# Performance work log

Measured on AMD Instinct MI355X. Metric: run time of the kernel, lower is better.

Reference implementation:

```python
import jax, jax.numpy as jnp
import numpy as np

B, L, H, NH, DH = 2, 4096, 768, 12, 64
W_ = 128          # one-sided sliding window
NL = 2            # encoder layers
VOCAB, OUT, FF = 50265, 384, 3072
EPS = 1e-5


def _ln(x, s, b):
    m = jnp.mean(x, axis=-1, keepdims=True)
    v = jnp.mean((x - m) ** 2, axis=-1, keepdims=True)
    return (x - m) / jnp.sqrt(v + EPS) * s + b


def _attn(x, amask, Wq, bq, Wk, bk, Wv, bv, Wo, bo):
    # x: [B,L,H]; sliding-window attention (one-sided W_) + global token 0
    def heads(Wt, bt):
        return (x @ Wt + bt).reshape(B, L, NH, DH).transpose(0, 2, 1, 3)  # [B,NH,L,DH]
    q, k, v = heads(Wq, bq), heads(Wk, bk), heads(Wv, bv)
    scale = 1.0 / np.sqrt(DH).astype(np.float32)
    C = W_
    nC = L // C
    qc = q.reshape(B, NH, nC, C, DH)

    def blocks(t):  # gather [prev, self, next] key chunks -> [B,NH,nC,3C,DH]
        tc = t.reshape(B, NH, nC, C, DH)
        tp = jnp.pad(tc, ((0, 0), (0, 0), (1, 1), (0, 0), (0, 0)))
        return jnp.concatenate([tp[:, :, :-2], tp[:, :, 1:-1], tp[:, :, 2:]], axis=3)

    k3, v3 = blocks(k), blocks(v)
    s_loc = jnp.einsum('bhncd,bhnkd->bhnck', qc, k3) * scale  # [B,NH,nC,C,3C]

    pos_k = (jnp.arange(nC)[:, None] - 1) * C + jnp.arange(3 * C)[None, :]  # [nC,3C]
    pos_q = jnp.arange(nC)[:, None] * C + jnp.arange(C)[None, :]            # [nC,C]
    within = jnp.abs(pos_q[:, :, None] - pos_k[:, None, :]) <= W_           # [nC,C,3C]
    valid = (pos_k >= 0) & (pos_k < L) & (pos_k != 0)  # key 0 handled as global column
    mk = amask[:, jnp.clip(pos_k, 0, L - 1)] > 0        # [B,nC,3C]
    m = within[None, None] & valid[None, None, :, None, :] & mk[:, None, :, None, :]
    s_loc = jnp.where(m, s_loc, -1e9)

    # every token also attends to the global token 0
    s_g = jnp.einsum('bhld,bhd->bhl', q, k[:, :, 0]) * scale  # [B,NH,L]
    s = jnp.concatenate([s_loc.reshape(B, NH, L, 3 * C), s_g[..., None]], axis=-1)
    p = jax.nn.softmax(s, axis=-1)
    p_loc = p[..., :3 * C].reshape(B, NH, nC, C, 3 * C)
    out = jnp.einsum('bhnck,bhnkd->bhncd', p_loc, v3).reshape(B, NH, L, DH)
    out = out + p[..., -1:] * v[:, :, 0][:, :, None, :]

    # global token 0 attends to everything
    s0 = jnp.einsum('bhd,bhld->bhl', q[:, :, 0], k) * scale
    s0 = jnp.where(amask[:, None, :] > 0, s0, -1e9)
    o0 = jnp.einsum('bhl,bhld->bhd', jax.nn.softmax(s0, axis=-1), v)
    out = out.at[:, :, 0, :].set(o0)

    out = out.transpose(0, 2, 1, 3).reshape(B, L, H)
    return out @ Wo + bo


def setup_inputs() -> dict:
    key = jax.random.key(0)
    ks = jax.random.split(key, 16)
    p = lambda k_, sh: 0.02 * jax.random.normal(k_, sh, jnp.float32)
    return {
        'input_ids': jax.random.randint(ks[0], (B, L), 0, VOCAB, dtype=jnp.int32),
        'attention_mask': jnp.ones((B, L), jnp.int32),
        'word_emb': p(ks[1], (VOCAB, H)),
        'pos_emb': p(ks[2], (L, H)),
        'emb_ln_s': jnp.ones((H,), jnp.float32), 'emb_ln_b': jnp.zeros((H,), jnp.float32),
        'Wq': p(ks[3], (NL, H, H)), 'bq': jnp.zeros((NL, H), jnp.float32),
        'Wk': p(ks[4], (NL, H, H)), 'bk': jnp.zeros((NL, H), jnp.float32),
        'Wv': p(ks[5], (NL, H, H)), 'bv': jnp.zeros((NL, H), jnp.float32),
        'Wo': p(ks[6], (NL, H, H)), 'bo': jnp.zeros((NL, H), jnp.float32),
        'ln1_s': jnp.ones((NL, H), jnp.float32), 'ln1_b': jnp.zeros((NL, H), jnp.float32),
        'W1': p(ks[7], (NL, H, FF)), 'b1': jnp.zeros((NL, FF), jnp.float32),
        'W2': p(ks[8], (NL, FF, H)), 'b2': jnp.zeros((NL, H), jnp.float32),
        'ln2_s': jnp.ones((NL, H), jnp.float32), 'ln2_b': jnp.zeros((NL, H), jnp.float32),
        'Wfc': p(ks[9], (H, OUT)), 'bfc': jnp.zeros((OUT,), jnp.float32),
    }


def reference(input_ids, attention_mask, word_emb, pos_emb, emb_ln_s, emb_ln_b,
              Wq, bq, Wk, bk, Wv, bv, Wo, bo, ln1_s, ln1_b,
              W1, b1, W2, b2, ln2_s, ln2_b, Wfc, bfc):
    x = word_emb[input_ids] + pos_emb[None]
    x = _ln(x, emb_ln_s, emb_ln_b)
    for l in range(NL):
        a = _attn(x, attention_mask, Wq[l], bq[l], Wk[l], bk[l], Wv[l], bv[l], Wo[l], bo[l])
        x = _ln(x + a, ln1_s[l], ln1_b[l])
        h = jax.nn.gelu(x @ W1[l] + b1[l])
        x = _ln(x + h @ W2[l] + b2[l], ln2_s[l], ln2_b[l])
    v_dn = x @ Wfc + bfc           # [B,L,OUT]
    cls = v_dn[:, 0]               # fc(last_hidden[:,0]) == v_dn[:,0]
    return v_dn, cls
```

## Files before the change

### kernel.cpp

```cpp
#include <hip/hip_runtime.h>
#include <hip/hip_bf16.h>
#include <stdint.h>

#define L_SEQ 4096
#define H_DIM 768
#define N_HEADS 12
#define D_HEAD 64
#define N_CHUNK 32
#define CHUNK 128
#define FF_DIM 3072
#define OUT_DIM 384
#define BATCH 2
#define EPS_LN 1e-5f
#define M_ROWS (BATCH * L_SEQ)
#define QKV_LD (3 * H_DIM)
#define NLOC (BATCH * N_HEADS * N_CHUNK)
#define NGSEG 8

typedef unsigned short u16;
typedef __bf16 bx8 __attribute__((ext_vector_type(8)));
typedef float fx4 __attribute__((ext_vector_type(4)));
typedef u16 ux8 __attribute__((ext_vector_type(8)));

__device__ __forceinline__ u16 f2bf(float f) {
  union { float f; unsigned u; } x; x.f = f;
  unsigned r = x.u + 0x7fffu + ((x.u >> 16) & 1u);
  return (u16)(r >> 16);
}
__device__ __forceinline__ float bf2f(u16 v) {
  union { unsigned u; float f; } x; x.u = ((unsigned)v) << 16;
  return x.f;
}

__device__ __forceinline__ void gload16(const void* g, void* l) {
  __builtin_amdgcn_global_load_lds((const __attribute__((address_space(1))) void*)g,
                                   (__attribute__((address_space(3))) void*)l, 16, 0, 0);
}

template<int OUT_BF16, int DO_GELU, int DO_CLS>
__global__ __launch_bounds__(256, 3)
void gemm_s(const u16* __restrict__ A, const u16* __restrict__ Bt,
            const float* __restrict__ bias,
            float* __restrict__ Cf, u16* __restrict__ Cb,
            float* __restrict__ cls,
            int N, int K)
{
  __shared__ __align__(16) u16 As[128 * 64];
  __shared__ __align__(16) u16 Bs[128 * 64];
  const int tid = threadIdx.x;
  const int lane = tid & 63, w = tid >> 6;
  const int c16 = lane & 15, g = lane >> 4;
  const int wr = w >> 1, wc = w & 1;

  const int nbn = N >> 7;
  int id = blockIdx.x;
  id = (id & 7) * (gridDim.x >> 3) + (id >> 3);
  const int bm = id / nbn, bn = id % nbn;

  const int srow = w * 8 + (lane >> 3);
  const int schunk = (lane & 7) ^ (lane >> 3);
  const u16* sA = A + (size_t)(bm * 128 + srow) * K + schunk * 8;
  const u16* sB = Bt + (size_t)(bn * 128 + srow) * K + schunk * 8;
  const int wdst = w * 512;

  fx4 acc[4][4] = {};

  for (int k0 = 0; k0 < K; k0 += 64) {
    #pragma unroll
    for (int i = 0; i < 4; i++) {
      gload16(sA + (size_t)(i * 32) * K + k0, &As[i * 2048 + wdst]);
      gload16(sB + (size_t)(i * 32) * K + k0, &Bs[i * 2048 + wdst]);
    }
    __syncthreads();
    #pragma unroll
    for (int h = 0; h < 2; h++) {
      bx8 af[4], bf[4];
      #pragma unroll
      for (int m = 0; m < 4; m++) {
        const int row = wr * 64 + m * 16 + c16;
        af[m] = *(const bx8*)&As[row * 64 + (((h << 2) + g) ^ (c16 & 7)) * 8];
      }
      #pragma unroll
      for (int n = 0; n < 4; n++) {
        const int row = wc * 64 + n * 16 + c16;
        bf[n] = *(const bx8*)&Bs[row * 64 + (((h << 2) + g) ^ (c16 & 7)) * 8];
      }
      #pragma unroll
      for (int m = 0; m < 4; m++)
        #pragma unroll
        for (int n = 0; n < 4; n++)
          acc[m][n] = __builtin_amdgcn_mfma_f32_16x16x32_bf16(af[m], bf[n], acc[m][n], 0, 0, 0);
    }
    __syncthreads();
  }

  const int row0 = bm * 128 + wr * 64 + g * 4;
  const int col0 = bn * 128 + wc * 64 + c16;
  #pragma unroll
  for (int n = 0; n < 4; n++) {
    const int col = col0 + n * 16;
    const float bb = bias[col];
    #pragma unroll
    for (int m = 0; m < 4; m++) {
      #pragma unroll
      for (int r = 0; r < 4; r++) {
        float y = acc[m][n][r] + bb;
        if (DO_GELU) {
          const float tt = y;
          y = 0.5f * tt * (1.0f + tanhf(0.7978845608f * (tt + 0.044715f * tt * tt * tt)));
        }
        const int row = row0 + m * 16 + r;
        const size_t idx = (size_t)row * N + col;
        if (OUT_BF16) Cb[idx] = f2bf(y);
        else Cf[idx] = y;
        if (DO_CLS) {
          if ((row & (L_SEQ - 1)) == 0)
            cls[(row >> 12) * OUT_DIM + col] = y;
        }
      }
    }
  }
}

#define P2_STR 64

__global__ __launch_bounds__(512, 2)
void attn_fused_kernel(const u16* __restrict__ qkv, const int* __restrict__ amask,
                       u16* __restrict__ attnout,
                       float* __restrict__ gpm, float* __restrict__ gps,
                       float* __restrict__ gpo)
{
  __shared__ __align__(16) u16 Klds[2][64 * 64];
  __shared__ __align__(16) u16 Vlds[2][64 * 64];
  __shared__ __align__(16) u16 Plds[8 * 16 * P2_STR];

  const int tid = threadIdx.x;
  const int lane = tid & 63, w = tid >> 6;

  if (blockIdx.x >= NLOC) {
    float* fsc = (float*)&Klds[0][0];
    float* qs  = fsc;
    float* es  = fsc + 64;
    float* red = fsc + 576;
    const int idx = blockIdx.x - NLOC;
    const int bh = idx >> 3, seg = idx & 7;
    const int b = bh / N_HEADS, h = bh % N_HEADS;
    const u16* base = qkv + (size_t)b * L_SEQ * QKV_LD + h * D_HEAD;

    if (tid < D_HEAD) qs[tid] = bf2f(base[tid]);
    __syncthreads();

    const int key = seg * 512 + tid;
    const ux8* kp = (const ux8*)(base + (size_t)key * QKV_LD + H_DIM);
    float dot = 0.f;
    #pragma unroll
    for (int i = 0; i < 8; i++) {
      const ux8 kv = kp[i];
      #pragma unroll
      for (int j = 0; j < 8; j++) dot += qs[i * 8 + j] * bf2f(kv[j]);
    }
    float sv = dot * 0.125f;
    if (amask[b * L_SEQ + key] == 0) sv = -1.0e9f;

    float mv = sv;
    #pragma unroll
    for (int off = 32; off > 0; off >>= 1) mv = fmaxf(mv, __shfl_xor(mv, off));
    if (lane == 0) red[w] = mv;
    __syncthreads();
    float M = -3.0e38f;
    #pragma unroll
    for (int i = 0; i < 8; i++) M = fmaxf(M, red[i]);

    const float e = __expf(sv - M);
    es[tid] = e;
    float s = e;
    #pragma unroll
    for (int off = 32; off > 0; off >>= 1) s += __shfl_xor(s, off);
    __syncthreads();
    if (lane == 0) red[w] = s;
    __syncthreads();
    float Sl = 0.f;
    #pragma unroll
    for (int i = 0; i < 8; i++) Sl += red[i];

    const int gi = tid >> 6, d = lane;
    const u16* vb = base + 2 * H_DIM + d;
    float acc = 0.f;
    #pragma unroll 4
    for (int i = 0; i < 64; i++) {
      const int kk = seg * 512 + gi * 64 + i;
      acc += es[gi * 64 + i] * bf2f(vb[(size_t)kk * QKV_LD]);
    }
    gpo[(((size_t)bh * NGSEG + seg) * 8 + gi) * D_HEAD + d] = acc;
    if (tid == 0) { gpm[bh * NGSEG + seg] = M; gps[bh * NGSEG + seg] = Sl; }
    return;
  }

  const int c16 = lane & 15, g = lane >> 4;
  const int bh = blockIdx.x >> 5;
  const int n = blockIdx.x & 31;
  const int b = bh / N_HEADS, h = bh % N_HEADS;

  const u16* qkvb = qkv + (size_t)b * L_SEQ * QKV_LD + h * D_HEAD;
  const int chunk_lo = n * CHUNK - CHUNK;

  const int qrow = n * CHUNK + w * 16 + c16;
  const u16* qp = qkvb + (size_t)qrow * QKV_LD + g * 8;
  const bx8 aq0 = *(const bx8*)qp;
  const bx8 aq1 = *(const bx8*)(qp + 32);

  unsigned kvm = 0;
  #pragma unroll
  for (int kf = 0; kf < 24; kf++) {
    const int pos = chunk_lo + kf * 16 + c16;
    bool ok = (pos >= 1) && (pos < L_SEQ);
    if (ok) ok = (amask[b * L_SEQ + pos] > 0);
    kvm |= ((unsigned)ok) << kf;
  }

  const int cq = w * 16 + g * 4;

  float m[4], l[4], pgv[4];
  {
    const u16* kp = qkvb + H_DIM + g * 8;
    const bx8 b0 = *(const bx8*)kp;
    const bx8 b1 = *(const bx8*)(kp + 32);
    fx4 sg = {};
    sg = __builtin_amdgcn_mfma_f32_16x16x32_bf16(aq0, b0, sg, 0, 0, 0);
    sg = __builtin_amdgcn_mfma_f32_16x16x32_bf16(aq1, b1, sg, 0, 0, 0);
    #pragma unroll
    for (int r = 0; r < 4; r++) {
      const float val = (c16 == 0) ? sg[r] * 0.125f : -1.0e9f;
      float mm = val;
      mm = fmaxf(mm, __shfl_xor(mm, 1));
      mm = fmaxf(mm, __shfl_xor(mm, 2));
      mm = fmaxf(mm, __shfl_xor(mm, 4));
      mm = fmaxf(mm, __shfl_xor(mm, 8));
      m[r] = mm;
      pgv[r] = __expf(val - mm);
      float t = pgv[r];
      t += __shfl_xor(t, 1);
      t += __shfl_xor(t, 2);
      t += __shfl_xor(t, 4);
      t += __shfl_xor(t, 8);
      l[r] = t;
    }
  }

  const int krow_s = w * 8 + (lane >> 3);
  const int ksc = (lane & 7) ^ (krow_s & 7);
  const int d = lane;
  const int vdst = d * 64 + ((w ^ (d & 7)) << 3);

  {
    int pos = chunk_lo + krow_s;
    if (pos < 0) pos = 0;
    if (pos >= L_SEQ) pos = L_SEQ - 1;
    gload16(qkvb + (size_t)pos * QKV_LD + H_DIM + ksc * 8, &Klds[0][w * 512]);
  }
  ux8 vreg;
  #pragma unroll
  for (int j = 0; j < 8; j++) {
    int pos = chunk_lo + w * 8 + j;
    if (pos < 0) pos = 0;
    if (pos >= L_SEQ) pos = L_SEQ - 1;
    vreg[j] = qkvb[(size_t)pos * QKV_LD + 2 * H_DIM + d];
  }
  *(ux8*)&Vlds[0][vdst] = vreg;
  __syncthreads();

  fx4 o[4] = {};
  u16* pb = Plds + w * 16 * P2_STR;
  const int prow = (w * 16 + c16) * P2_STR;

  for (int t = 0; t < 6; t++) {
    const int cur = t & 1, nxt = cur ^ 1;

    if (t < 5) {
      int pos = chunk_lo + (t + 1) * 64 + krow_s;
      if (pos < 0) pos = 0;
      if (pos >= L_SEQ) pos = L_SEQ - 1;
      gload16(qkvb + (size_t)pos * QKV_LD + H_DIM + ksc * 8, &Klds[nxt][w * 512]);
      #pragma unroll
      for (int j = 0; j < 8; j++) {
        int vp = chunk_lo + (t + 1) * 64 + w * 8 + j;
        if (vp < 0) vp = 0;
        if (vp >= L_SEQ) vp = L_SEQ - 1;
        vreg[j] = qkvb[(size_t)vp * QKV_LD + 2 * H_DIM + d];
      }
    }

    fx4 s[4];
    __builtin_amdgcn_s_setprio(1);
    #pragma unroll
    for (int kf = 0; kf < 4; kf++) {
      const int krow = kf * 16 + c16;
      const bx8 b0 = *(const bx8*)&Klds[cur][krow * 64 + ((g ^ (c16 & 7)) << 3)];
      const bx8 b1 = *(const bx8*)&Klds[cur][krow * 64 + (((4 + g) ^ (c16 & 7)) << 3)];
      fx4 a = {};
      a = __builtin_amdgcn_mfma_f32_16x16x32_bf16(aq0, b0, a, 0, 0, 0);
      a = __builtin_amdgcn_mfma_f32_16x16x32_bf16(aq1, b1, a, 0, 0, 0);
      s[kf] = a;
    }
    __builtin_amdgcn_s_setprio(0);
    float pmax[4];
    #pragma unroll
    for (int r = 0; r < 4; r++) pmax[r] = -3.0e38f;
    #pragma unroll
    for (int kf = 0; kf < 4; kf++) {
      const int KF = t * 4 + kf;
      const int j = KF * 16 + c16;
      const bool kv = ((kvm >> KF) & 1u) != 0;
      #pragma unroll
      for (int r = 0; r < 4; r++) {
        const int c = cq + r;
        const bool keep = kv && (j >= c && j <= c + 256);
        const float val = keep ? s[kf][r] * 0.125f : -1.0e9f;
        s[kf][r] = val;
        pmax[r] = fmaxf(pmax[r], val);
      }
    }
    #pragma unroll
    for (int r = 0; r < 4; r++) {
      float mm = pmax[r];
      mm = fmaxf(mm, __shfl_xor(mm, 1));
      mm = fmaxf(mm, __shfl_xor(mm, 2));
      mm = fmaxf(mm, __shfl_xor(mm, 4));
      mm = fmaxf(mm, __shfl_xor(mm, 8));
      const float newm = fmaxf(m[r], mm);
      const float scale = __expf(m[r] - newm);
      m[r] = newm;
      l[r] *= scale;
      pgv[r] *= scale;
      #pragma unroll
      for (int df = 0; df < 4; df++) o[df][r] *= scale;
    }
    float lsum[4] = {0.f, 0.f, 0.f, 0.f};
    #pragma unroll
    for (int kf = 0; kf < 4; kf++)
      #pragma unroll
      for (int r = 0; r < 4; r++) {
        const float p = __expf(s[kf][r] - m[r]);
        s[kf][r] = p;
        lsum[r] += p;
      }
    #pragma unroll
    for (int r = 0; r < 4; r++) {
      float tt = lsum[r];
      tt += __shfl_xor(tt, 1);
      tt += __shfl_xor(tt, 2);
      tt += __shfl_xor(tt, 4);
      tt += __shfl_xor(tt, 8);
      l[r] += tt;
    }
    #pragma unroll
    for (int kf = 0; kf < 4; kf++) {
      #pragma unroll
      for (int r = 0; r < 4; r++) {
        const int rr = g * 4 + r;
        const int jj = kf * 16 + c16;
        pb[rr * P2_STR + (((jj >> 3) ^ (rr & 7)) << 3) + (jj & 7)] = f2bf(s[kf][r]);
      }
    }
    __builtin_amdgcn_s_setprio(1);
    #pragma unroll
    for (int kt = 0; kt < 2; kt++) {
      const int ckp = kt * 4 + g;
      const bx8 pa = *(const bx8*)&Plds[prow + ((ckp ^ (c16 & 7)) << 3)];
      #pragma unroll
      for (int df = 0; df < 4; df++) {
        const int vrow = df * 16 + c16;
        const bx8 vvf = *(const bx8*)&Vlds[cur][vrow * 64 + ((ckp ^ (c16 & 7)) << 3)];
        o[df] = __builtin_amdgcn_mfma_f32_16x16x32_bf16(pa, vvf, o[df], 0, 0, 0);
      }
    }
    __builtin_amdgcn_s_setprio(0);
    if (t < 5) *(ux8*)&Vlds[nxt][vdst] = vreg;
    __syncthreads();
  }

  float rinv[4], pg[4];
  #pragma unroll
  for (int r = 0; r < 4; r++) {
    rinv[r] = 1.0f / l[r];
    pg[r] = __shfl(pgv[r], g * 16);
  }
  u16* ob = attnout + (size_t)b * L_SEQ * H_DIM + h * D_HEAD;
  const int posq = n * CHUNK + w * 16 + g * 4;
  #pragma unroll
  for (int df = 0; df < 4; df++) {
    const float v0f = bf2f(qkvb[2 * H_DIM + df * 16 + c16]);
    #pragma unroll
    for (int r = 0; r < 4; r++)
      ob[(size_t)(posq + r) * H_DIM + df * 16 + c16] =
          f2bf((o[df][r] + pg[r] * v0f) * rinv[r]);
  }
}

__global__ __launch_bounds__(64)
void attn_g_combine(const float* __restrict__ gpm, const float* __restrict__ gps,
                    const float* __restrict__ gpo, u16* __restrict__ attnout)
{
  const int bh = blockIdx.x;
  const int b = bh / N_HEADS, h = bh % N_HEADS;
  const int d = threadIdx.x;
  float M = -3.0e38f;
  #pragma unroll
  for (int s = 0; s < NGSEG; s++) M = fmaxf(M, gpm[bh * NGSEG + s]);
  float S = 0.f, acc = 0.f;
  #pragma unroll
  for (int s = 0; s < NGSEG; s++) {
    const float sc = __expf(gpm[bh * NGSEG + s] - M);
    S += gps[bh * NGSEG + s] * sc;
    #pragma unroll
    for (int gi = 0; gi < 8; gi++)
      acc += gpo[(((size_t)bh * NGSEG + s) * 8 + gi) * D_HEAD + d] * sc;
  }
  attnout[(size_t)b * L_SEQ * H_DIM + h * D_HEAD + d] = f2bf(acc / S);
}

__device__ __forceinline__ void block_stats(float sum, float sq, float* red,
                                            float& mean, float& rstd)
{
  const int lane = threadIdx.x & 63, wv = threadIdx.x >> 6;
  #pragma unroll
  for (int off = 32; off > 0; off >>= 1) {
    sum += __shfl_xor(sum, off);
    sq  += __shfl_xor(sq, off);
  }
  if (lane == 0) { red[wv] = sum; red[4 + wv] = sq; }
  __syncthreads();
  sum = red[0] + red[1] + red[2] + red[3];
  sq  = red[4] + red[5] + red[6] + red[7];
  mean = sum * (1.0f / H_DIM);
  const float var = sq * (1.0f / H_DIM) - mean * mean;
  rstd = rsqrtf(var + EPS_LN);
}

__global__ __launch_bounds__(256)
void add_ln_kernel(u16* xio, const u16* __restrict__ yin,
                   const float* __restrict__ gam, const float* __restrict__ bet)
{
  __shared__ float red[8];
  const int row = blockIdx.x, tid = threadIdx.x;
  float v[3]; float sum = 0.f, sq = 0.f;
  #pragma unroll
  for (int i = 0; i < 3; i++) {
    const int c = tid + i * 256;
    const float t = bf2f(xio[(size_t)row * H_DIM + c]) + bf2f(yin[(size_t)row * H_DIM + c]);
    v[i] = t; sum += t; sq += t * t;
  }
  float mean, rstd;
  block_stats(sum, sq, red, mean, rstd);
  #pragma unroll
  for (int i = 0; i < 3; i++) {
    const int c = tid + i * 256;
    const float y = (v[i] - mean) * rstd * gam[c] + bet[c];
    xio[(size_t)row * H_DIM + c] = f2bf(y);
  }
}

__global__ __launch_bounds__(256)
void prep_embed(const float* __restrict__ Wq, const float* __restrict__ Wk,
                const float* __restrict__ Wv, const float* __restrict__ Wo,
                const float* __restrict__ W1, const float* __restrict__ W2,
                const float* __restrict__ Wfc,
                const float* __restrict__ bq, const float* __restrict__ bk,
                const float* __restrict__ bv,
                u16* __restrict__ wqkvT, u16* __restrict__ woT,
                u16* __restrict__ w1T, u16* __restrict__ w2T,
                u16* __restrict__ wfcT, float* __restrict__ bqkv,
                const int* __restrict__ ids, const float* __restrict__ wemb,
                const float* __restrict__ pemb, const float* __restrict__ gam,
                const float* __restrict__ bet, u16* __restrict__ xb)
{
  const int t = blockIdx.x;
  const int tid = threadIdx.x;
  __shared__ float tile[32][33];

  if (t >= 14130) {
    const int row = t - 14130;
    const int l = row & (L_SEQ - 1);
    const int id = ids[row];
    float v[3]; float sum = 0.f, sq = 0.f;
    #pragma unroll
    for (int i = 0; i < 3; i++) {
      const int c = tid + i * 256;
      const float x = wemb[(size_t)id * H_DIM + c] + pemb[(size_t)l * H_DIM + c];
      v[i] = x; sum += x; sq += x * x;
    }
    float mean, rstd;
    block_stats(sum, sq, &tile[0][0], mean, rstd);
    #pragma unroll
    for (int i = 0; i < 3; i++) {
      const int c = tid + i * 256;
      const float y = (v[i] - mean) * rstd * gam[c] + bet[c];
      xb[(size_t)row * H_DIM + c] = f2bf(y);
    }
    return;
  }
  if (t >= 14112) {
    const int idx = t - 14112;
    const int l = idx / 9, j = idx % 9;
    const int i = j * 256 + tid;
    if (i < H_DIM)          bqkv[l * QKV_LD + i] = bq[l * H_DIM + i];
    else if (i < 2 * H_DIM) bqkv[l * QKV_LD + i] = bk[l * H_DIM + i - H_DIM];
    else if (i < 3 * H_DIM) bqkv[l * QKV_LD + i] = bv[l * H_DIM + i - 2 * H_DIM];
    return;
  }
  const float* src; u16* dst; int K, N, r;
  if (t < 13824) {
    const int l = t / 6912; r = t % 6912;
    if (r < 2304) {
      const int mq = r / 576; r = r % 576; K = H_DIM; N = H_DIM;
      if (mq == 0)      src = Wq + (size_t)l * H_DIM * H_DIM;
      else if (mq == 1) src = Wk + (size_t)l * H_DIM * H_DIM;
      else if (mq == 2) src = Wv + (size_t)l * H_DIM * H_DIM;
      else              src = Wo + (size_t)l * H_DIM * H_DIM;
      dst = (mq < 3) ? wqkvT + (size_t)l * QKV_LD * H_DIM + (size_t)mq * H_DIM * H_DIM
                     : woT + (size_t)l * H_DIM * H_DIM;
    } else if (r < 4608) {
      r -= 2304; K = H_DIM; N = FF_DIM;
      src = W1 + (size_t)l * H_DIM * FF_DIM;
      dst = w1T + (size_t)l * FF_DIM * H_DIM;
    } else {
      r -= 4608; K = FF_DIM; N = H_DIM;
      src = W2 + (size_t)l * FF_DIM * H_DIM;
      dst = w2T + (size_t)l * H_DIM * FF_DIM;
    }
  } else {
    r = t - 13824; K = H_DIM; N = OUT_DIM; src = Wfc; dst = wfcT;
  }
  const int ntn = N >> 5;
  const int k0 = (r / ntn) * 32, n0 = (r % ntn) * 32;
  const int tx = tid & 31, ty = tid >> 5;
  #pragma unroll
  for (int i = 0; i < 32; i += 8)
    tile[ty + i][tx] = src[(size_t)(k0 + ty + i) * N + n0 + tx];
  __syncthreads();
  #pragma unroll
  for (int i = 0; i < 32; i += 8)
    dst[(size_t)(n0 + ty + i) * K + k0 + tx] = f2bf(tile[tx][ty + i]);
}

extern "C" void kernel_launch(void* const* d_in, const int* in_sizes, int n_in,
                              void* d_out, int out_size, void* d_ws, size_t ws_size,
                              hipStream_t stream)
{
  (void)in_sizes; (void)n_in; (void)out_size; (void)ws_size;
  const int*   ids   = (const int*)d_in[0];
  const int*   amask = (const int*)d_in[1];
  const float* wemb  = (const float*)d_in[2];
  const float* pemb  = (const float*)d_in[3];
  const float* elns  = (const float*)d_in[4];
  const float* elnb  = (const float*)d_in[5];
  const float* Wq    = (const float*)d_in[6];
  const float* bq    = (const float*)d_in[7];
  const float* Wk    = (const float*)d_in[8];
  const float* bk    = (const float*)d_in[9];
  const float* Wv    = (const float*)d_in[10];
  const float* bv    = (const float*)d_in[11];
  const float* Wo    = (const float*)d_in[12];
  const float* bo    = (const float*)d_in[13];
  const float* ln1s  = (const float*)d_in[14];
  const float* ln1b  = (const float*)d_in[15];
  const float* W1    = (const float*)d_in[16];
  const float* b1    = (const float*)d_in[17];
  const float* W2    = (const float*)d_in[18];
  const float* b2    = (const float*)d_in[19];
  const float* ln2s  = (const float*)d_in[20];
  const float* ln2b  = (const float*)d_in[21];
  const float* Wfc   = (const float*)d_in[22];
  const float* bfc   = (const float*)d_in[23];

  char* ws = (char*)d_ws;
  size_t off = 0;
  auto alloc = [&](size_t bytes) -> void* {
    void* p = ws + off;
    off += (bytes + 255) & ~(size_t)255;
    return p;
  };
  u16* xb     = (u16*)alloc((size_t)M_ROWS * H_DIM * 2);
  u16* projb  = (u16*)alloc((size_t)M_ROWS * H_DIM * 2);
  u16* big    = (u16*)alloc((size_t)M_ROWS * FF_DIM * 2);
  u16* attno  = (u16*)alloc((size_t)M_ROWS * H_DIM * 2);
  u16* wqkvT  = (u16*)alloc((size_t)2 * QKV_LD * H_DIM * 2);
  u16* woT    = (u16*)alloc((size_t)2 * H_DIM * H_DIM * 2);
  u16* w1T    = (u16*)alloc((size_t)2 * FF_DIM * H_DIM * 2);
  u16* w2T    = (u16*)alloc((size_t)2 * H_DIM * FF_DIM * 2);
  u16* wfcT   = (u16*)alloc((size_t)OUT_DIM * H_DIM * 2);
  float* bqkv = (float*)alloc(2 * QKV_LD * 4);
  float* gpm  = (float*)alloc((size_t)BATCH * N_HEADS * NGSEG * 4);
  float* gps  = (float*)alloc((size_t)BATCH * N_HEADS * NGSEG * 4);
  float* gpo  = (float*)alloc((size_t)BATCH * N_HEADS * NGSEG * 8 * D_HEAD * 4);

  u16* qkvb = big;
  u16* ff1  = big;

  prep_embed<<<14130 + M_ROWS, 256, 0, stream>>>(
      Wq, Wk, Wv, Wo, W1, W2, Wfc, bq, bk, bv,
      wqkvT, woT, w1T, w2T, wfcT, bqkv,
      ids, wemb, pemb, elns, elnb, xb);

  for (int l = 0; l < 2; l++) {
    gemm_s<1, 0, 0><<<(M_ROWS / 128) * (QKV_LD / 128), 256, 0, stream>>>(
        xb, wqkvT + (size_t)l * QKV_LD * H_DIM, bqkv + l * QKV_LD,
        nullptr, qkvb, nullptr, QKV_LD, H_DIM);
    attn_fused_kernel<<<NLOC + BATCH * N_HEADS * NGSEG, 512, 0, stream>>>(
        qkvb, amask, attno, gpm, gps, gpo);
    attn_g_combine<<<BATCH * N_HEADS, 64, 0, stream>>>(gpm, gps, gpo, attno);
    gemm_s<1, 0, 0><<<(M_ROWS / 128) * (H_DIM / 128), 256, 0, stream>>>(
        attno, woT + (size_t)l * H_DIM * H_DIM, bo + l * H_DIM,
        nullptr, projb, nullptr, H_DIM, H_DIM);
    add_ln_kernel<<<M_ROWS, 256, 0, stream>>>(xb, projb, ln1s + l * H_DIM, ln1b + l * H_DIM);
    gemm_s<1, 1, 0><<<(M_ROWS / 128) * (FF_DIM / 128), 256, 0, stream>>>(
        xb, w1T + (size_t)l * FF_DIM * H_DIM, b1 + l * FF_DIM,
        nullptr, ff1, nullptr, FF_DIM, H_DIM);
    gemm_s<1, 0, 0><<<(M_ROWS / 128) * (H_DIM / 128), 256, 0, stream>>>(
        ff1, w2T + (size_t)l * H_DIM * FF_DIM, b2 + l * H_DIM,
        nullptr, projb, nullptr, H_DIM, FF_DIM);
    add_ln_kernel<<<M_ROWS, 256, 0, stream>>>(xb, projb, ln2s + l * H_DIM, ln2b + l * H_DIM);
  }

  float* vdn = (float*)d_out;
  float* cls = vdn + (size_t)BATCH * L_SEQ * OUT_DIM;
  gemm_s<0, 0, 1><<<(M_ROWS / 128) * (OUT_DIM / 128), 256, 0, stream>>>(
      xb, wfcT, bfc, vdn, nullptr, cls, OUT_DIM, H_DIM);
}
```

Measured before the change: 591.8 us.

## Split fused attention and prep kernels, raise GEMM occupancy hint

```diff
diff --git a/kernel.cpp b/kernel.cpp
--- a/kernel.cpp
+++ b/kernel.cpp
@@ -14,7 +14,6 @@
 #define EPS_LN 1e-5f
 #define M_ROWS (BATCH * L_SEQ)
 #define QKV_LD (3 * H_DIM)
-#define NLOC (BATCH * N_HEADS * N_CHUNK)
 #define NGSEG 8
 
 typedef unsigned short u16;
@@ -38,7 +37,7 @@
 }
 
 template<int OUT_BF16, int DO_GELU, int DO_CLS>
-__global__ __launch_bounds__(256, 3)
+__global__ __launch_bounds__(256, 4)
 void gemm_s(const u16* __restrict__ A, const u16* __restrict__ Bt,
             const float* __restrict__ bias,
             float* __restrict__ Cf, u16* __restrict__ Cb,
@@ -125,10 +124,8 @@
 #define P2_STR 64
 
 __global__ __launch_bounds__(512, 2)
-void attn_fused_kernel(const u16* __restrict__ qkv, const int* __restrict__ amask,
-                       u16* __restrict__ attnout,
-                       float* __restrict__ gpm, float* __restrict__ gps,
-                       float* __restrict__ gpo)
+void attn_local_kernel(const u16* __restrict__ qkv, const int* __restrict__ amask,
+                       u16* __restrict__ attnout)
 {
   __shared__ __align__(16) u16 Klds[2][64 * 64];
   __shared__ __align__(16) u16 Vlds[2][64 * 64];
@@ -136,67 +133,8 @@
 
   const int tid = threadIdx.x;
   const int lane = tid & 63, w = tid >> 6;
-
-  if (blockIdx.x >= NLOC) {
-    float* fsc = (float*)&Klds[0][0];
-    float* qs  = fsc;
-    float* es  = fsc + 64;
-    float* red = fsc + 576;
-    const int idx = blockIdx.x - NLOC;
-    const int bh = idx >> 3, seg = idx & 7;
-    const int b = bh / N_HEADS, h = bh % N_HEADS;
-    const u16* base = qkv + (size_t)b * L_SEQ * QKV_LD + h * D_HEAD;
-
-    if (tid < D_HEAD) qs[tid] = bf2f(base[tid]);
-    __syncthreads();
-
-    const int key = seg * 512 + tid;
-    const ux8* kp = (const ux8*)(base + (size_t)key * QKV_LD + H_DIM);
-    float dot = 0.f;
-    #pragma unroll
-    for (int i = 0; i < 8; i++) {
-      const ux8 kv = kp[i];
-      #pragma unroll
-      for (int j = 0; j < 8; j++) dot += qs[i * 8 + j] * bf2f(kv[j]);
-    }
-    float sv = dot * 0.125f;
-    if (amask[b * L_SEQ + key] == 0) sv = -1.0e9f;
-
-    float mv = sv;
-    #pragma unroll
-    for (int off = 32; off > 0; off >>= 1) mv = fmaxf(mv, __shfl_xor(mv, off));
-    if (lane == 0) red[w] = mv;
-    __syncthreads();
-    float M = -3.0e38f;
-    #pragma unroll
-    for (int i = 0; i < 8; i++) M = fmaxf(M, red[i]);
-
-    const float e = __expf(sv - M);
-    es[tid] = e;
-    float s = e;
-    #pragma unroll
-    for (int off = 32; off > 0; off >>= 1) s += __shfl_xor(s, off);
-    __syncthreads();
-    if (lane == 0) red[w] = s;
-    __syncthreads();
-    float Sl = 0.f;
-    #pragma unroll
-    for (int i = 0; i < 8; i++) Sl += red[i];
-
-    const int gi = tid >> 6, d = lane;
-    const u16* vb = base + 2 * H_DIM + d;
-    float acc = 0.f;
-    #pragma unroll 4
-    for (int i = 0; i < 64; i++) {
-      const int kk = seg * 512 + gi * 64 + i;
-      acc += es[gi * 64 + i] * bf2f(vb[(size_t)kk * QKV_LD]);
-    }
-    gpo[(((size_t)bh * NGSEG + seg) * 8 + gi) * D_HEAD + d] = acc;
-    if (tid == 0) { gpm[bh * NGSEG + seg] = M; gps[bh * NGSEG + seg] = Sl; }
-    return;
-  }
-
   const int c16 = lane & 15, g = lane >> 4;
+
   const int bh = blockIdx.x >> 5;
   const int n = blockIdx.x & 31;
   const int b = bh / N_HEADS, h = bh % N_HEADS;
@@ -397,6 +335,69 @@
   }
 }
 
+__global__ __launch_bounds__(512)
+void attn_g_split(const u16* __restrict__ qkv, const int* __restrict__ amask,
+                  float* __restrict__ gpm, float* __restrict__ gps,
+                  float* __restrict__ gpo)
+{
+  __shared__ float qs[D_HEAD];
+  __shared__ float es[512];
+  __shared__ float red[8];
+  const int tid = threadIdx.x;
+  const int lane = tid & 63, w = tid >> 6;
+  const int idx = blockIdx.x;
+  const int bh = idx >> 3, seg = idx & 7;
+  const int b = bh / N_HEADS, h = bh % N_HEADS;
+  const u16* base = qkv + (size_t)b * L_SEQ * QKV_LD + h * D_HEAD;
+
+  if (tid < D_HEAD) qs[tid] = bf2f(base[tid]);
+  __syncthreads();
+
+  const int key = seg * 512 + tid;
+  const ux8* kp = (const ux8*)(base + (size_t)key * QKV_LD + H_DIM);
+  float dot = 0.f;
+  #pragma unroll
+  for (int i = 0; i < 8; i++) {
+    const ux8 kv = kp[i];
+    #pragma unroll
+    for (int j = 0; j < 8; j++) dot += qs[i * 8 + j] * bf2f(kv[j]);
+  }
+  float sv = dot * 0.125f;
+  if (amask[b * L_SEQ + key] == 0) sv = -1.0e9f;
+
+  float mv = sv;
+  #pragma unroll
+  for (int off = 32; off > 0; off >>= 1) mv = fmaxf(mv, __shfl_xor(mv, off));
+  if (lane == 0) red[w] = mv;
+  __syncthreads();
+  float M = -3.0e38f;
+  #pragma unroll
+  for (int i = 0; i < 8; i++) M = fmaxf(M, red[i]);
+
+  const float e = __expf(sv - M);
+  es[tid] = e;
+  float s = e;
+  #pragma unroll
+  for (int off = 32; off > 0; off >>= 1) s += __shfl_xor(s, off);
+  __syncthreads();
+  if (lane == 0) red[w] = s;
+  __syncthreads();
+  float Sl = 0.f;
+  #pragma unroll
+  for (int i = 0; i < 8; i++) Sl += red[i];
+
+  const int gi = tid >> 6, d = lane;
+  const u16* vb = base + 2 * H_DIM + d;
+  float acc = 0.f;
+  #pragma unroll 4
+  for (int i = 0; i < 64; i++) {
+    const int kk = seg * 512 + gi * 64 + i;
+    acc += es[gi * 64 + i] * bf2f(vb[(size_t)kk * QKV_LD]);
+  }
+  gpo[(((size_t)bh * NGSEG + seg) * 8 + gi) * D_HEAD + d] = acc;
+  if (tid == 0) { gpm[bh * NGSEG + seg] = M; gps[bh * NGSEG + seg] = Sl; }
+}
+
 __global__ __launch_bounds__(64)
 void attn_g_combine(const float* __restrict__ gpm, const float* __restrict__ gps,
                     const float* __restrict__ gpo, u16* __restrict__ attnout)
@@ -438,6 +439,32 @@
 }
 
 __global__ __launch_bounds__(256)
+void embed_ln_kernel(const int* __restrict__ ids, const float* __restrict__ wemb,
+                     const float* __restrict__ pemb, const float* __restrict__ gam,
+                     const float* __restrict__ bet, u16* __restrict__ xb)
+{
+  __shared__ float red[8];
+  const int row = blockIdx.x, tid = threadIdx.x;
+  const int l = row & (L_SEQ - 1);
+  const int id = ids[row];
+  float v[3]; float sum = 0.f, sq = 0.f;
+  #pragma unroll
+  for (int i = 0; i < 3; i++) {
+    const int c = tid + i * 256;
+    const float t = wemb[(size_t)id * H_DIM + c] + pemb[(size_t)l * H_DIM + c];
+    v[i] = t; sum += t; sq += t * t;
+  }
+  float mean, rstd;
+  block_stats(sum, sq, red, mean, rstd);
+  #pragma unroll
+  for (int i = 0; i < 3; i++) {
+    const int c = tid + i * 256;
+    const float y = (v[i] - mean) * rstd * gam[c] + bet[c];
+    xb[(size_t)row * H_DIM + c] = f2bf(y);
+  }
+}
+
+__global__ __launch_bounds__(256)
 void add_ln_kernel(u16* xio, const u16* __restrict__ yin,
                    const float* __restrict__ gam, const float* __restrict__ bet)
 {
@@ -461,44 +488,18 @@
 }
 
 __global__ __launch_bounds__(256)
-void prep_embed(const float* __restrict__ Wq, const float* __restrict__ Wk,
-                const float* __restrict__ Wv, const float* __restrict__ Wo,
-                const float* __restrict__ W1, const float* __restrict__ W2,
-                const float* __restrict__ Wfc,
-                const float* __restrict__ bq, const float* __restrict__ bk,
-                const float* __restrict__ bv,
-                u16* __restrict__ wqkvT, u16* __restrict__ woT,
-                u16* __restrict__ w1T, u16* __restrict__ w2T,
-                u16* __restrict__ wfcT, float* __restrict__ bqkv,
-                const int* __restrict__ ids, const float* __restrict__ wemb,
-                const float* __restrict__ pemb, const float* __restrict__ gam,
-                const float* __restrict__ bet, u16* __restrict__ xb)
+void prep_weights(const float* __restrict__ Wq, const float* __restrict__ Wk,
+                  const float* __restrict__ Wv, const float* __restrict__ Wo,
+                  const float* __restrict__ W1, const float* __restrict__ W2,
+                  const float* __restrict__ Wfc,
+                  const float* __restrict__ bq, const float* __restrict__ bk,
+                  const float* __restrict__ bv,
+                  u16* __restrict__ wqkvT, u16* __restrict__ woT,
+                  u16* __restrict__ w1T, u16* __restrict__ w2T,
+                  u16* __restrict__ wfcT, float* __restrict__ bqkv)
 {
   const int t = blockIdx.x;
   const int tid = threadIdx.x;
-  __shared__ float tile[32][33];
-
-  if (t >= 14130) {
-    const int row = t - 14130;
-    const int l = row & (L_SEQ - 1);
-    const int id = ids[row];
-    float v[3]; float sum = 0.f, sq = 0.f;
-    #pragma unroll
-    for (int i = 0; i < 3; i++) {
-      const int c = tid + i * 256;
-      const float x = wemb[(size_t)id * H_DIM + c] + pemb[(size_t)l * H_DIM + c];
-      v[i] = x; sum += x; sq += x * x;
-    }
-    float mean, rstd;
-    block_stats(sum, sq, &tile[0][0], mean, rstd);
-    #pragma unroll
-    for (int i = 0; i < 3; i++) {
-      const int c = tid + i * 256;
-      const float y = (v[i] - mean) * rstd * gam[c] + bet[c];
-      xb[(size_t)row * H_DIM + c] = f2bf(y);
-    }
-    return;
-  }
   if (t >= 14112) {
     const int idx = t - 14112;
     const int l = idx / 9, j = idx % 9;
@@ -512,13 +513,13 @@
   if (t < 13824) {
     const int l = t / 6912; r = t % 6912;
     if (r < 2304) {
-      const int mq = r / 576; r = r % 576; K = H_DIM; N = H_DIM;
-      if (mq == 0)      src = Wq + (size_t)l * H_DIM * H_DIM;
-      else if (mq == 1) src = Wk + (size_t)l * H_DIM * H_DIM;
-      else if (mq == 2) src = Wv + (size_t)l * H_DIM * H_DIM;
-      else              src = Wo + (size_t)l * H_DIM * H_DIM;
-      dst = (mq < 3) ? wqkvT + (size_t)l * QKV_LD * H_DIM + (size_t)mq * H_DIM * H_DIM
-                     : woT + (size_t)l * H_DIM * H_DIM;
+      const int m = r / 576; r = r % 576; K = H_DIM; N = H_DIM;
+      if (m == 0)      src = Wq + (size_t)l * H_DIM * H_DIM;
+      else if (m == 1) src = Wk + (size_t)l * H_DIM * H_DIM;
+      else if (m == 2) src = Wv + (size_t)l * H_DIM * H_DIM;
+      else             src = Wo + (size_t)l * H_DIM * H_DIM;
+      dst = (m < 3) ? wqkvT + (size_t)l * QKV_LD * H_DIM + (size_t)m * H_DIM * H_DIM
+                    : woT + (size_t)l * H_DIM * H_DIM;
     } else if (r < 4608) {
       r -= 2304; K = H_DIM; N = FF_DIM;
       src = W1 + (size_t)l * H_DIM * FF_DIM;
@@ -533,6 +534,7 @@
   }
   const int ntn = N >> 5;
   const int k0 = (r / ntn) * 32, n0 = (r % ntn) * 32;
+  __shared__ float tile[32][33];
   const int tx = tid & 31, ty = tid >> 5;
   #pragma unroll
   for (int i = 0; i < 32; i += 8)
@@ -597,17 +599,17 @@
   u16* qkvb = big;
   u16* ff1  = big;
 
-  prep_embed<<<14130 + M_ROWS, 256, 0, stream>>>(
-      Wq, Wk, Wv, Wo, W1, W2, Wfc, bq, bk, bv,
-      wqkvT, woT, w1T, w2T, wfcT, bqkv,
-      ids, wemb, pemb, elns, elnb, xb);
+  prep_weights<<<14130, 256, 0, stream>>>(Wq, Wk, Wv, Wo, W1, W2, Wfc,
+                                          bq, bk, bv,
+                                          wqkvT, woT, w1T, w2T, wfcT, bqkv);
+  embed_ln_kernel<<<M_ROWS, 256, 0, stream>>>(ids, wemb, pemb, elns, elnb, xb);
 
   for (int l = 0; l < 2; l++) {
     gemm_s<1, 0, 0><<<(M_ROWS / 128) * (QKV_LD / 128), 256, 0, stream>>>(
         xb, wqkvT + (size_t)l * QKV_LD * H_DIM, bqkv + l * QKV_LD,
         nullptr, qkvb, nullptr, QKV_LD, H_DIM);
-    attn_fused_kernel<<<NLOC + BATCH * N_HEADS * NGSEG, 512, 0, stream>>>(
-        qkvb, amask, attno, gpm, gps, gpo);
+    attn_local_kernel<<<BATCH * N_HEADS * N_CHUNK, 512, 0, stream>>>(qkvb, amask, attno);
+    attn_g_split<<<BATCH * N_HEADS * NGSEG, 512, 0, stream>>>(qkvb, amask, gpm, gps, gpo);
     attn_g_combine<<<BATCH * N_HEADS, 64, 0, stream>>>(gpm, gps, gpo, attno);
     gemm_s<1, 0, 0><<<(M_ROWS / 128) * (H_DIM / 128), 256, 0, stream>>>(
         attno, woT + (size_t)l * H_DIM * H_DIM, bo + l * H_DIM,
```

Result: faster. 555.7 us (-6.1%).
